# Optimization experiments

Measured on AMD Instinct MI355X. Metric: run time of the kernel, lower is better.

Reference implementation:

```python
import jax, jax.numpy as jnp
import numpy as np

C, C_H, N_HEAD = 8, 1, 8
B, S, I = 1, 4096, 1024


def setup_inputs() -> dict:
    key = jax.random.key(0)
    ks = jax.random.split(key, 8)
    m = jax.random.normal(ks[0], (B, S, I, C), dtype=jnp.float32)
    mask = jnp.ones((B, S, I), dtype=jnp.float32)
    sc = 0.1
    return {
        "m": m,
        "mask": mask,
        "ln_gamma": jnp.ones((C,), jnp.float32),
        "ln_beta": jnp.zeros((C,), jnp.float32),
        "Wq": jax.random.normal(ks[1], (C, C_H * N_HEAD), jnp.float32) * sc,
        "Wk": jax.random.normal(ks[2], (C, C_H), jnp.float32) * sc,
        "Wv": jax.random.normal(ks[3], (C, C_H), jnp.float32) * sc,
        "Wg": jax.random.normal(ks[4], (C, C_H * N_HEAD), jnp.float32) * sc,
        "bg": jax.random.normal(ks[5], (C_H * N_HEAD,), jnp.float32) * sc,
        "Wo": jax.random.normal(ks[6], (C_H * N_HEAD, C), jnp.float32) * sc,
        "bo": jax.random.normal(ks[7], (C,), jnp.float32) * sc,
    }


def reference(m, mask, ln_gamma, ln_beta, Wq, Wk, Wv, Wg, bg, Wo, bo):
    # m: (B, s, i, c) -> work in (B, i, s, c); mask: (B, s, i) -> (B, i, s)
    mt = jnp.swapaxes(m, -2, -3)
    mk = jnp.swapaxes(mask, -1, -2)
    c_h = Wk.shape[1]
    h = Wq.shape[1] // c_h
    Bz, iz, sz, _ = mt.shape

    # LayerNorm over channel dim (eps=1e-5, population variance)
    mu = jnp.mean(mt, axis=-1, keepdims=True)
    var = jnp.mean(jnp.square(mt - mu), axis=-1, keepdims=True)
    mn = (mt - mu) / jnp.sqrt(var + 1e-5) * ln_gamma + ln_beta  # (B,i,s,c)

    # Masked mean pool over sequences -> global query per residue column
    q = jnp.sum(mn * mk[..., None], axis=-2) / (jnp.sum(mk, axis=-1)[..., None] + 1e-5)  # (B,i,c)

    q = (q @ Wq) * (c_h ** -0.5)          # (B,i,h*c_h)
    k = mn @ Wk                           # (B,i,s,c_h)  shared across heads
    v = mn @ Wv                           # (B,i,s,c_h)
    g = jax.nn.sigmoid(mn @ Wg + bg)      # (B,i,s,h*c_h)

    q = q.reshape(Bz, iz, h, c_h)
    g = g.reshape(Bz, iz, sz, h, c_h)

    bias = 1e9 * (mk - 1.0)               # (B,i,s)
    a = jnp.einsum('bihd,bisd->bihs', q, k) + bias[..., None, :]
    a = jax.nn.softmax(a, axis=-1)        # (B,i,h,s)
    o = jnp.einsum('bihs,bisd->bihd', a, v)  # (B,i,h,c_h)

    o = o[..., None, :, :] * g            # (B,i,s,h,c_h) gated, broadcast over s
    o = o.reshape(Bz, iz, sz, h * c_h) @ Wo + bo  # (B,i,s,c)
    return jnp.swapaxes(o, -2, -3)        # (B,s,i,c)
```

## Files before the change

kernel.cpp:

```cpp
#include <hip/hip_runtime.h>

#define I_LEN 1024

__device__ __forceinline__ float bf2f(unsigned int lo16) {
  unsigned int u = lo16 << 16;
  float f; __builtin_memcpy(&f, &u, 4); return f;
}
__device__ __forceinline__ unsigned int f2bf(float f) {
  unsigned int u; __builtin_memcpy(&u, &f, 4);
  return (u + 0x7FFFu + ((u >> 16) & 1u)) >> 16;
}

__global__ __launch_bounds__(1024) void msa_k1(
    const float* __restrict__ m, const float* __restrict__ mask,
    const float* __restrict__ lng, const float* __restrict__ lnb,
    const float* __restrict__ Wq, const float* __restrict__ Wk,
    const float* __restrict__ Wv, float* __restrict__ o_tab)
{
  __shared__ unsigned int kvs[4096 * 4];
  __shared__ float red[16][4][16];
  __shared__ float fin[4][9];
  __shared__ float qtab[4][8];

  const int t    = threadIdx.x;
  const int col  = t & 3;
  const int r    = t >> 2;
  const int lane = t & 63;
  const int wave = t >> 6;
  const int icol = blockIdx.x * 4 + col;

  float swk = 0.f, swv = 0.f, kb = 0.f, vb = 0.f;
#pragma unroll
  for (int c = 0; c < 8; ++c) {
    swk = fmaf(lng[c], Wk[c], swk);  swv = fmaf(lng[c], Wv[c], swv);
    kb  = fmaf(lnb[c], Wk[c], kb);   vb  = fmaf(lnb[c], Wv[c], vb);
  }

  unsigned int mb = 0;
  float qnx[8] = {0,0,0,0,0,0,0,0};
  float qd = 0.0f;

#pragma unroll 2
  for (int j = 0; j < 16; ++j) {
    const int s = r + 256 * j;
    const float4* mp = (const float4*)(m + (size_t)(s * I_LEN + icol) * 8);
    float4 lo = mp[0], hi = mp[1];
    const float mk = mask[s * I_LEN + icol];
    float x[8] = {lo.x, lo.y, lo.z, lo.w, hi.x, hi.y, hi.z, hi.w};
    float su = 0.f, s2 = 0.f;
#pragma unroll
    for (int c = 0; c < 8; ++c) { su += x[c]; s2 = fmaf(x[c], x[c], s2); }
    const float mu   = su * 0.125f;
    const float var  = s2 * 0.125f - mu * mu;
    const float rstd = rsqrtf(var + 1e-5f);
    float dk = 0.f, dv = 0.f;
#pragma unroll
    for (int c = 0; c < 8; ++c) {
      const float xg = x[c] * lng[c];
      dk = fmaf(xg, Wk[c], dk);
      dv = fmaf(xg, Wv[c], dv);
      x[c] = xg;
    }
    const float kk  = fmaf(rstd, fmaf(-mu, swk, dk), kb);
    const float vv  = fmaf(rstd, fmaf(-mu, swv, dv), vb);
    const float mr  = mk * rstd;
    const float mmr = -mu * mr;
#pragma unroll
    for (int c = 0; c < 8; ++c)
      qnx[c] = fmaf(x[c], mr, fmaf(lng[c], mmr, qnx[c]));
    qd += mk;
    kvs[s * 4 + col] = (f2bf(kk) << 16) | f2bf(vv);
    mb |= (mk > 0.5f ? 1u : 0u) << j;
  }

#pragma unroll
  for (int q = 0; q < 9; ++q) {
    float x = (q < 8) ? qnx[q] : qd;
#pragma unroll
    for (int off = 4; off <= 32; off <<= 1) x += __shfl_xor(x, off, 64);
    if (lane < 4) red[wave][lane][q] = x;
  }
  __syncthreads();
  if (t < 36) {
    int cc = t / 9, q = t - cc * 9;
    float s = 0.f;
#pragma unroll
    for (int w = 0; w < 16; ++w) s += red[w][cc][q];
    fin[cc][q] = s;
  }
  __syncthreads();
  if (t < 32) {
    int cc = t >> 3, h = t & 7;
    const float invd = 1.0f / (fin[cc][8] + 1e-5f);
    float qv = 0.f;
#pragma unroll
    for (int c = 0; c < 8; ++c) {
      const float qn = fmaf(lnb[c], fin[cc][8], fin[cc][c]);
      qv = fmaf(qn * invd, Wq[c * 8 + h], qv);
    }
    qtab[cc][h] = qv;
  }
  __syncthreads();

  float qh[8];
#pragma unroll
  for (int h = 0; h < 8; ++h) qh[h] = qtab[col][h];

  float se[8] = {0,0,0,0,0,0,0,0};
  float sv[8] = {0,0,0,0,0,0,0,0};
#pragma unroll 4
  for (int j = 0; j < 16; ++j) {
    const unsigned int w = kvs[(r + 256 * j) * 4 + col];
    const float kk = bf2f(w >> 16);
    const float vv = bf2f(w & 0xFFFFu);
    const float on = ((mb >> j) & 1u) ? 1.0f : 0.0f;
#pragma unroll
    for (int h = 0; h < 8; ++h) {
      const float e = __expf(qh[h] * kk) * on;
      se[h] += e;
      sv[h] = fmaf(e, vv, sv[h]);
    }
  }
#pragma unroll
  for (int q = 0; q < 16; ++q) {
    float x = (q < 8) ? se[q] : sv[q - 8];
#pragma unroll
    for (int off = 4; off <= 32; off <<= 1) x += __shfl_xor(x, off, 64);
    if (lane < 4) red[wave][lane][q] = x;
  }
  __syncthreads();
  if (t < 32) {
    int cc = t >> 3, h = t & 7;
    float a = 0.f, b = 0.f;
#pragma unroll
    for (int w = 0; w < 16; ++w) { a += red[w][cc][h]; b += red[w][cc][8 + h]; }
    o_tab[(blockIdx.x * 4 + cc) * 8 + h] = b / a;
  }
}

__global__ __launch_bounds__(256, 2) void msa_k2(
    const float* __restrict__ m,
    const float* __restrict__ lng, const float* __restrict__ lnb,
    const float* __restrict__ Wg, const float* __restrict__ bg,
    const float* __restrict__ Wo, const float* __restrict__ bo,
    const float* __restrict__ o_tab, float* __restrict__ out)
{
  const int tid = blockIdx.x * 256 + threadIdx.x;
  const int i = tid & (I_LEN - 1);

  float sgv[8], tbv[8];
#pragma unroll
  for (int h = 0; h < 8; ++h) {
    float s = 0.f, tb = bg[h];
#pragma unroll
    for (int c = 0; c < 8; ++c) {
      s  = fmaf(lng[c], Wg[c * 8 + h], s);
      tb = fmaf(lnb[c], Wg[c * 8 + h], tb);
    }
    sgv[h] = s; tbv[h] = tb;
  }

  const float4* op = (const float4*)(o_tab + i * 8);
  const float4 o1 = op[0], o2 = op[1];
  const float A[8] = {o1.x, o1.y, o1.z, o1.w, o2.x, o2.y, o2.z, o2.w};

#pragma unroll 2
  for (int q = 0; q < 8; ++q) {
    const size_t p = (size_t)tid + (size_t)q * 524288;
    const float4* mp = (const float4*)(m + p * 8);
    const float4 lo = mp[0], hi = mp[1];
    float x[8] = {lo.x, lo.y, lo.z, lo.w, hi.x, hi.y, hi.z, hi.w};
    float su = 0.f, s2 = 0.f;
#pragma unroll
    for (int c = 0; c < 8; ++c) { su += x[c]; s2 = fmaf(x[c], x[c], s2); }
    const float mu   = su * 0.125f;
    const float var  = s2 * 0.125f - mu * mu;
    const float rstd = rsqrtf(var + 1e-5f);
#pragma unroll
    for (int c = 0; c < 8; ++c) x[c] *= lng[c];
    float acc[8];
#pragma unroll
    for (int c = 0; c < 8; ++c) acc[c] = bo[c];
#pragma unroll
    for (int h = 0; h < 8; ++h) {
      float d = 0.f;
#pragma unroll
      for (int c = 0; c < 8; ++c) d = fmaf(x[c], Wg[c * 8 + h], d);
      const float gl = fmaf(rstd, fmaf(-mu, sgv[h], d), tbv[h]);
      const float gv = A[h] / (1.0f + __expf(-gl));
#pragma unroll
      for (int c = 0; c < 8; ++c) acc[c] = fmaf(gv, Wo[h * 8 + c], acc[c]);
    }
    float4* outp = (float4*)(out + p * 8);
    outp[0] = make_float4(acc[0], acc[1], acc[2], acc[3]);
    outp[1] = make_float4(acc[4], acc[5], acc[6], acc[7]);
  }
}

extern "C" void kernel_launch(void* const* d_in, const int* in_sizes, int n_in,
                              void* d_out, int out_size, void* d_ws, size_t ws_size,
                              hipStream_t stream) {
  const float* m    = (const float*)d_in[0];
  const float* mask = (const float*)d_in[1];
  const float* lng  = (const float*)d_in[2];
  const float* lnb  = (const float*)d_in[3];
  const float* Wq   = (const float*)d_in[4];
  const float* Wk   = (const float*)d_in[5];
  const float* Wv   = (const float*)d_in[6];
  const float* Wg   = (const float*)d_in[7];
  const float* bg   = (const float*)d_in[8];
  const float* Wo   = (const float*)d_in[9];
  const float* bo   = (const float*)d_in[10];
  float* out   = (float*)d_out;
  float* o_tab = (float*)d_ws;

  hipLaunchKernelGGL(msa_k1, dim3(256), dim3(1024), 0, stream,
                     m, mask, lng, lnb, Wq, Wk, Wv, o_tab);
  hipLaunchKernelGGL(msa_k2, dim3(2048), dim3(256), 0, stream,
                     m, lng, lnb, Wg, bg, Wo, bo, o_tab, out);
}
```

Baseline: 307.9 us.

## Split pooled-attention pass into coalesced row-chunk pass and per-column reduction pass

The first kernel now assigns one thread per residue column and one block per 8-row chunk of sequences, so reads of m are fully coalesced across a row. It writes bf16 K/V in a transposed layout, per-chunk partial pooled sums and mask bytes to workspace. A new second kernel reduces the partials per column, forms the query and computes the softmax-weighted values. The old design used 4 columns per block with strided row reads and only 256 blocks. The change adds workspace traffic of about 16MB K/V plus 24MB of partials and an extra launch. The output kernel also switches to nontemporal stores.

```diff
diff --git a/kernel.cpp b/kernel.cpp
--- a/kernel.cpp
+++ b/kernel.cpp
@@ -1,6 +1,11 @@
 #include <hip/hip_runtime.h>
 
 #define I_LEN 1024
+#define S_LEN 4096
+#define CHUNKS 512
+#define ROWS 8
+
+typedef float f32x4 __attribute__((ext_vector_type(4)));
 
 __device__ __forceinline__ float bf2f(unsigned int lo16) {
   unsigned int u = lo16 << 16;
@@ -11,23 +16,16 @@
   return (u + 0x7FFFu + ((u >> 16) & 1u)) >> 16;
 }
 
-__global__ __launch_bounds__(1024) void msa_k1(
+__global__ __launch_bounds__(1024, 4) void msa_k1a(
     const float* __restrict__ m, const float* __restrict__ mask,
     const float* __restrict__ lng, const float* __restrict__ lnb,
-    const float* __restrict__ Wq, const float* __restrict__ Wk,
-    const float* __restrict__ Wv, float* __restrict__ o_tab)
+    const float* __restrict__ Wk, const float* __restrict__ Wv,
+    unsigned int* __restrict__ kvT, float* __restrict__ part,
+    unsigned char* __restrict__ mbytes)
 {
-  __shared__ unsigned int kvs[4096 * 4];
-  __shared__ float red[16][4][16];
-  __shared__ float fin[4][9];
-  __shared__ float qtab[4][8];
-
-  const int t    = threadIdx.x;
-  const int col  = t & 3;
-  const int r    = t >> 2;
-  const int lane = t & 63;
-  const int wave = t >> 6;
-  const int icol = blockIdx.x * 4 + col;
+  const int i  = threadIdx.x;
+  const int ch = blockIdx.x;
+  const int s0 = ch * ROWS;
 
   float swk = 0.f, swv = 0.f, kb = 0.f, vb = 0.f;
 #pragma unroll
@@ -36,16 +34,17 @@
     kb  = fmaf(lnb[c], Wk[c], kb);   vb  = fmaf(lnb[c], Wv[c], vb);
   }
 
+  float qnx[8] = {0,0,0,0,0,0,0,0};
+  float qd = 0.f;
+  unsigned int kvbuf[ROWS];
   unsigned int mb = 0;
-  float qnx[8] = {0,0,0,0,0,0,0,0};
-  float qd = 0.0f;
 
 #pragma unroll 2
-  for (int j = 0; j < 16; ++j) {
-    const int s = r + 256 * j;
-    const float4* mp = (const float4*)(m + (size_t)(s * I_LEN + icol) * 8);
-    float4 lo = mp[0], hi = mp[1];
-    const float mk = mask[s * I_LEN + icol];
+  for (int j = 0; j < ROWS; ++j) {
+    const int s = s0 + j;
+    const float4* mp = (const float4*)(m + (size_t)(s * I_LEN + i) * 8);
+    const float4 lo = mp[0], hi = mp[1];
+    const float mk = mask[s * I_LEN + i];
     float x[8] = {lo.x, lo.y, lo.z, lo.w, hi.x, hi.y, hi.z, hi.w};
     float su = 0.f, s2 = 0.f;
 #pragma unroll
@@ -69,51 +68,81 @@
     for (int c = 0; c < 8; ++c)
       qnx[c] = fmaf(x[c], mr, fmaf(lng[c], mmr, qnx[c]));
     qd += mk;
-    kvs[s * 4 + col] = (f2bf(kk) << 16) | f2bf(vv);
+    kvbuf[j] = (f2bf(kk) << 16) | f2bf(vv);
     mb |= (mk > 0.5f ? 1u : 0u) << j;
   }
 
+  uint4* kp = (uint4*)(kvT + (size_t)i * S_LEN + s0);
+  kp[0] = make_uint4(kvbuf[0], kvbuf[1], kvbuf[2], kvbuf[3]);
+  kp[1] = make_uint4(kvbuf[4], kvbuf[5], kvbuf[6], kvbuf[7]);
+
+  float4* pp = (float4*)(part + ((size_t)ch * I_LEN + i) * 12);
+  pp[0] = make_float4(qnx[0], qnx[1], qnx[2], qnx[3]);
+  pp[1] = make_float4(qnx[4], qnx[5], qnx[6], qnx[7]);
+  pp[2] = make_float4(qd, 0.f, 0.f, 0.f);
+
+  mbytes[(size_t)i * CHUNKS + ch] = (unsigned char)mb;
+}
+
+__global__ __launch_bounds__(256) void msa_k1b(
+    const float* __restrict__ lnb, const float* __restrict__ Wq,
+    const unsigned int* __restrict__ kvT, const float* __restrict__ part,
+    const unsigned char* __restrict__ mbytes, float* __restrict__ o_tab)
+{
+  __shared__ float red[4][16];
+  __shared__ float qp_s[8];
+  __shared__ float qtab[8];
+
+  const int i    = blockIdx.x;
+  const int t    = threadIdx.x;
+  const int lane = t & 63;
+  const int wave = t >> 6;
+
+  float v[9];
+  {
+    const float4* p0 = (const float4*)(part + ((size_t)t         * I_LEN + i) * 12);
+    const float4* p1 = (const float4*)(part + ((size_t)(t + 256) * I_LEN + i) * 12);
+    const float4 a0 = p0[0], a1 = p0[1], a2 = p0[2];
+    const float4 b0 = p1[0], b1 = p1[1], b2 = p1[2];
+    v[0] = a0.x + b0.x; v[1] = a0.y + b0.y; v[2] = a0.z + b0.z; v[3] = a0.w + b0.w;
+    v[4] = a1.x + b1.x; v[5] = a1.y + b1.y; v[6] = a1.z + b1.z; v[7] = a1.w + b1.w;
+    v[8] = a2.x + b2.x;
+  }
 #pragma unroll
   for (int q = 0; q < 9; ++q) {
-    float x = (q < 8) ? qnx[q] : qd;
-#pragma unroll
-    for (int off = 4; off <= 32; off <<= 1) x += __shfl_xor(x, off, 64);
-    if (lane < 4) red[wave][lane][q] = x;
-  }
-  __syncthreads();
-  if (t < 36) {
-    int cc = t / 9, q = t - cc * 9;
-    float s = 0.f;
-#pragma unroll
-    for (int w = 0; w < 16; ++w) s += red[w][cc][q];
-    fin[cc][q] = s;
-  }
-  __syncthreads();
-  if (t < 32) {
-    int cc = t >> 3, h = t & 7;
-    const float invd = 1.0f / (fin[cc][8] + 1e-5f);
+    float x = v[q];
+#pragma unroll
+    for (int off = 1; off <= 32; off <<= 1) x += __shfl_xor(x, off, 64);
+    if (lane == 0) red[wave][q] = x;
+  }
+  __syncthreads();
+  if (t < 8) {
+    const float d = red[0][8] + red[1][8] + red[2][8] + red[3][8];
+    const float s = red[0][t] + red[1][t] + red[2][t] + red[3][t];
+    qp_s[t] = (s + lnb[t] * d) / (d + 1e-5f);
+  }
+  __syncthreads();
+  if (t < 8) {
     float qv = 0.f;
 #pragma unroll
-    for (int c = 0; c < 8; ++c) {
-      const float qn = fmaf(lnb[c], fin[cc][8], fin[cc][c]);
-      qv = fmaf(qn * invd, Wq[c * 8 + h], qv);
-    }
-    qtab[cc][h] = qv;
-  }
-  __syncthreads();
-
+    for (int c = 0; c < 8; ++c) qv = fmaf(qp_s[c], Wq[c * 8 + t], qv);
+    qtab[t] = qv;
+  }
+  __syncthreads();
   float qh[8];
 #pragma unroll
-  for (int h = 0; h < 8; ++h) qh[h] = qtab[col][h];
+  for (int h = 0; h < 8; ++h) qh[h] = qtab[h];
 
   float se[8] = {0,0,0,0,0,0,0,0};
   float sv[8] = {0,0,0,0,0,0,0,0};
 #pragma unroll 4
   for (int j = 0; j < 16; ++j) {
-    const unsigned int w = kvs[(r + 256 * j) * 4 + col];
+    const int s = t + 256 * j;
+    const unsigned int w = kvT[(size_t)i * S_LEN + s];
+    const unsigned int mbit = (mbytes[(size_t)i * CHUNKS + (s >> 3)] >> (s & 7)) & 1u;
     const float kk = bf2f(w >> 16);
     const float vv = bf2f(w & 0xFFFFu);
-    const float on = ((mb >> j) & 1u) ? 1.0f : 0.0f;
+    const float on = mbit ? 1.0f : 0.0f;
 #pragma unroll
     for (int h = 0; h < 8; ++h) {
       const float e = __expf(qh[h] * kk) * on;
@@ -125,16 +154,14 @@
   for (int q = 0; q < 16; ++q) {
     float x = (q < 8) ? se[q] : sv[q - 8];
 #pragma unroll
-    for (int off = 4; off <= 32; off <<= 1) x += __shfl_xor(x, off, 64);
-    if (lane < 4) red[wave][lane][q] = x;
-  }
-  __syncthreads();
-  if (t < 32) {
-    int cc = t >> 3, h = t & 7;
-    float a = 0.f, b = 0.f;
-#pragma unroll
-    for (int w = 0; w < 16; ++w) { a += red[w][cc][h]; b += red[w][cc][8 + h]; }
-    o_tab[(blockIdx.x * 4 + cc) * 8 + h] = b / a;
+    for (int off = 1; off <= 32; off <<= 1) x += __shfl_xor(x, off, 64);
+    if (lane == 0) red[wave][q] = x;
+  }
+  __syncthreads();
+  if (t < 8) {
+    const float a = red[0][t]     + red[1][t]     + red[2][t]     + red[3][t];
+    const float b = red[0][8 + t] + red[1][8 + t] + red[2][8 + t] + red[3][8 + t];
+    o_tab[(size_t)i * 8 + t] = b / a;
   }
 }
 
@@ -191,9 +218,11 @@
 #pragma unroll
       for (int c = 0; c < 8; ++c) acc[c] = fmaf(gv, Wo[h * 8 + c], acc[c]);
     }
-    float4* outp = (float4*)(out + p * 8);
-    outp[0] = make_float4(acc[0], acc[1], acc[2], acc[3]);
-    outp[1] = make_float4(acc[4], acc[5], acc[6], acc[7]);
+    f32x4* outp = (f32x4*)(out + p * 8);
+    f32x4 r0 = {acc[0], acc[1], acc[2], acc[3]};
+    f32x4 r1 = {acc[4], acc[5], acc[6], acc[7]};
+    __builtin_nontemporal_store(r0, outp);
+    __builtin_nontemporal_store(r1, outp + 1);
   }
 }
 
@@ -211,11 +240,18 @@
   const float* bg   = (const float*)d_in[8];
   const float* Wo   = (const float*)d_in[9];
   const float* bo   = (const float*)d_in[10];
-  float* out   = (float*)d_out;
-  float* o_tab = (float*)d_ws;
-
-  hipLaunchKernelGGL(msa_k1, dim3(256), dim3(1024), 0, stream,
-                     m, mask, lng, lnb, Wq, Wk, Wv, o_tab);
+  float* out = (float*)d_out;
+
+  char* ws = (char*)d_ws;
+  float*         o_tab  = (float*)ws;
+  unsigned int*  kvT    = (unsigned int*)(ws + ((size_t)1 << 20));
+  float*         part   = (float*)(ws + ((size_t)20 << 20));
+  unsigned char* mbytes = (unsigned char*)(ws + ((size_t)48 << 20));
+
+  hipLaunchKernelGGL(msa_k1a, dim3(CHUNKS), dim3(1024), 0, stream,
+                     m, mask, lng, lnb, Wk, Wv, kvT, part, mbytes);
+  hipLaunchKernelGGL(msa_k1b, dim3(I_LEN), dim3(256), 0, stream,
+                     lnb, Wq, kvT, part, mbytes, o_tab);
   hipLaunchKernelGGL(msa_k2, dim3(2048), dim3(256), 0, stream,
                      m, lng, lnb, Wg, bg, Wo, bo, o_tab, out);
 }
```

Result: slower. 329.4 us (+7.0%).
